# Performance work log

Measured on AMD Instinct MI355X. Metric: run time of the kernel, lower is better.

The kernel has to match this reference:

```python
import jax, jax.numpy as jnp
import numpy as np
import itertools as it
from math import factorial

DIM, N = 3, 30
K = 2 * DIM * N + 1          # 181
P = factorial(N) // factorial(N - DIM)  # 24360
DEMB = DIM * DIM + K         # 190

# permutation index tables (trace-time constants)
_combs = np.array(list(it.permutations(range(N), DIM)), dtype=np.int32)          # (P, DIM)
_rest = np.array([sorted(set(range(N)) - set(map(int, c))) for c in _combs],
                 dtype=np.int32)                                                  # (P, N-DIM)


def setup_inputs() -> dict:
    key = jax.random.key(0)
    k0, k1, k2, k3, k4 = jax.random.split(key, 5)
    return {
        "matrix": jax.random.normal(k0, (DIM, N), dtype=jnp.float32),
        "Ws_in": jax.random.normal(k1, (K, DIM), dtype=jnp.float32),        # inner weights_sort
        "Wd_in": jax.random.normal(k2, (K, N - DIM), dtype=jnp.float32),    # inner weights_dot
        "Ws_out": jax.random.normal(k3, (K, DEMB), dtype=jnp.float32),      # outer weights_sort
        "Wd_out": jax.random.normal(k4, (K, P), dtype=jnp.float32),         # outer weights_dot
    }


def reference(matrix, Ws_in, Wd_in, Ws_out, Wd_out):
    combs = jnp.asarray(_combs)   # (P, DIM)
    rest = jnp.asarray(_rest)     # (P, N-DIM)
    cols = matrix.T               # (N, DIM) -- columns of the cloud as rows

    # UpperGram, batched over all P permutations
    Xd = cols[combs].transpose(0, 2, 1)   # (P, DIM, DIM) selected columns
    Xr = cols[rest].transpose(0, 2, 1)    # (P, DIM, N-DIM) remaining columns (sorted)
    gram = jnp.einsum('pdi,pdj->pij', Xd, Xd)          # Xd^T Xd, (P, DIM, DIM)
    # torch flattens gram.transpose(1,0); gram is exactly symmetric so this equals row-major
    gram_flat = gram.transpose(0, 2, 1).reshape(P, DIM * DIM)
    proj = jnp.einsum('pdi,pdm->pim', Xd, Xr)          # Xd^T Xrest, (P, DIM, N-DIM)

    # inner Embed (non-original branch), batched over P
    sm = jnp.einsum('pim,ki->pmk', proj, Ws_in)        # (P, N-DIM, K)
    sm_sorted = jnp.sort(sm, axis=1)                   # column-wise sort (dim=0 in torch)
    emb = jnp.einsum('km,pmk->pk', Wd_in, sm_sorted)   # diag(Wd @ sorted), (P, K)

    vec = jnp.concatenate([gram_flat, emb], axis=1)    # (P, DEMB); torch's vec before .t()

    # outer Embed (original branch) on mat = vec.T (DEMB, P)
    sm2 = vec @ Ws_out.T                               # mat^T @ Ws^T, (P, K)
    sm2_sorted = jnp.sort(sm2, axis=0)                 # sort over permutation axis
    out = jnp.einsum('kp,pk->k', Wd_out, sm2_sorted)   # diag(Wd @ sorted), (K,)
    return out
```

## Files before the change

kernel.cpp:

```cpp
#include <hip/hip_runtime.h>
#include <hip/hip_bf16.h>

#define DIMK 3
#define NPTS 30
#define KK   181
#define PP   24360
#define DEMB 190
#define VLD  192
#define SNP  24576

typedef __attribute__((ext_vector_type(8))) short bf16x8;
typedef __attribute__((ext_vector_type(4))) float f32x4;
typedef __attribute__((ext_vector_type(2))) __fp16 h2;
typedef __attribute__((ext_vector_type(4))) ushort u16x4;

__device__ __forceinline__ ushort f2bf(float f) {
    unsigned u = __float_as_uint(f);
    u += 0x7FFFu + ((u >> 16) & 1u);
    return (ushort)(u >> 16);
}

__global__ __launch_bounds__(1024, 2) void k_inner(
    const float* __restrict__ M,
    const float* __restrict__ Ws_in,
    const float* __restrict__ Wd_in,
    const float* __restrict__ Wout,
    ushort* __restrict__ Abf,
    ushort* __restrict__ vec)
{
    __shared__ float Gs[NPTS * 32];
    __shared__ float WsS[192 * 3];
    __shared__ float WdS[192 * 28];

    const int tid = threadIdx.x;

    {
        int gid = blockIdx.x * 1024 + tid;
        if (gid < 192 * 192) {
            int k = gid / 192, d = gid - k * 192;
            Abf[gid] = (k < KK && d < DEMB) ? f2bf(Wout[k * DEMB + d]) : (ushort)0;
        }
    }

    for (int i = tid; i < 192 * 3; i += 1024) WsS[i] = (i < KK * 3) ? Ws_in[i] : 0.f;
    for (int i = tid; i < 192 * 28; i += 1024) {
        int k = i / 28, m = i - k * 28;
        WdS[i] = (k < KK && m < 27) ? Wd_in[k * 27 + m] : 0.f;
    }
    for (int e = tid; e < NPTS * 32; e += 1024) {
        int a = e >> 5, b = e & 31;
        Gs[e] = (b < NPTS)
            ? (M[a] * M[b] + M[NPTS + a] * M[NPTS + b] + M[2 * NPTS + a] * M[2 * NPTS + b])
            : 0.f;
    }
    __syncthreads();

    const int wave = __builtin_amdgcn_readfirstlane(tid >> 6);
    const int lane = tid & 63;
    const int wid = blockIdx.x * 16 + wave;
    const int chunk = wid % 3;
    const int pstream = wid / 3;
    const int nstream = (chunk == 2) ? 2730 : 2731;
    const int k = chunk * 64 + lane;

    const float INF = __builtin_inff();
    const bool kvalid = (k < KK);
    const float w0 = WsS[k * 3 + 0];
    const float w1 = WsS[k * 3 + 1];
    const float w2 = WsS[k * 3 + 2];
    const float* wd = WdS + k * 28;

    const int NPAIR = PP / 2;

    for (int t = pstream; t < NPAIR; t += nstream) {
        const int p0 = 2 * t;
        int i0 = p0 / 812;
        int r  = p0 - i0 * 812;
        int i1 = r / 28;
        int i2 = r - i1 * 28;
        int c0 = i0;
        int c1 = i1 + (i1 >= c0 ? 1 : 0);
        int lo = min(c0, c1), hi = max(c0, c1);
        int c2a = i2;
        if (c2a >= lo) c2a++;
        if (c2a >= hi) c2a++;
        int c2b = i2 + 1;
        if (c2b >= lo) c2b++;
        if (c2b >= hi) c2b++;

        ushort* vrow0 = vec + (long)p0 * VLD;
        ushort* vrow1 = vrow0 + VLD;

        if (chunk == 0 && lane < 9) {
            int i = lane / 3, j = lane % 3;
            int cia = (i == 0) ? c0 : ((i == 1) ? c1 : c2a);
            int cja = (j == 0) ? c0 : ((j == 1) ? c1 : c2a);
            vrow0[lane] = f2bf(Gs[(cia << 5) + cja]);
            int cib = (i == 0) ? c0 : ((i == 1) ? c1 : c2b);
            int cjb = (j == 0) ? c0 : ((j == 1) ? c1 : c2b);
            vrow1[lane] = f2bf(Gs[(cib << 5) + cjb]);
        }

        const float* g0 = Gs + (c0 << 5);
        const float* g1 = Gs + (c1 << 5);
        const float* ga = Gs + (c2a << 5);
        const float* gb = Gs + (c2b << 5);
        const unsigned basem = (1u << c0) | (1u << c1);
        const unsigned maska = basem | (1u << c2a);
        const unsigned maskb = basem | (1u << c2b);

        h2 s[30];
#pragma unroll
        for (int q = 0; q < 8; ++q) {
            float4 x0 = *(const float4*)&g0[q * 4];
            float4 x1 = *(const float4*)&g1[q * 4];
            float4 xa = *(const float4*)&ga[q * 4];
            float4 xb = *(const float4*)&gb[q * 4];
            int j0 = q * 4;
            if (j0 + 0 < NPTS) {
                float c = w0 * x0.x + w1 * x1.x;
                float va = w2 * xa.x + c;
                float vb = w2 * xb.x + c;
                va = ((maska >> (j0 + 0)) & 1u) ? INF : va;
                vb = ((maskb >> (j0 + 0)) & 1u) ? INF : vb;
                s[j0 + 0] = __builtin_amdgcn_cvt_pkrtz(va, vb);
            }
            if (j0 + 1 < NPTS) {
                float c = w0 * x0.y + w1 * x1.y;
                float va = w2 * xa.y + c;
                float vb = w2 * xb.y + c;
                va = ((maska >> (j0 + 1)) & 1u) ? INF : va;
                vb = ((maskb >> (j0 + 1)) & 1u) ? INF : vb;
                s[j0 + 1] = __builtin_amdgcn_cvt_pkrtz(va, vb);
            }
            if (j0 + 2 < NPTS) {
                float c = w0 * x0.z + w1 * x1.z;
                float va = w2 * xa.z + c;
                float vb = w2 * xb.z + c;
                va = ((maska >> (j0 + 2)) & 1u) ? INF : va;
                vb = ((maskb >> (j0 + 2)) & 1u) ? INF : vb;
                s[j0 + 2] = __builtin_amdgcn_cvt_pkrtz(va, vb);
            }
            if (j0 + 3 < NPTS) {
                float c = w0 * x0.w + w1 * x1.w;
                float va = w2 * xa.w + c;
                float vb = w2 * xb.w + c;
                va = ((maska >> (j0 + 3)) & 1u) ? INF : va;
                vb = ((maskb >> (j0 + 3)) & 1u) ? INF : vb;
                s[j0 + 3] = __builtin_amdgcn_cvt_pkrtz(va, vb);
            }
        }

#pragma unroll
        for (int pw = 1; pw < 32; pw <<= 1) {
#pragma unroll
            for (int kk = pw; kk >= 1; kk >>= 1) {
#pragma unroll
                for (int j = kk % pw; j + kk < 32; j += 2 * kk) {
#pragma unroll
                    for (int i = 0; i < kk; ++i) {
                        int a = i + j, b = i + j + kk;
                        if (a / (pw * 2) == b / (pw * 2) && b < 30
                            && !(pw == 16 && a == 27)) {
                            h2 x = s[a], y = s[b];
                            s[a] = __builtin_elementwise_min(x, y);
                            s[b] = __builtin_elementwise_max(x, y);
                        }
                    }
                }
            }
        }

        if (kvalid) {
            float emb0 = 0.f, emb1 = 0.f;
#pragma unroll
            for (int j = 0; j < 24; j += 4) {
                float4 w4 = *(const float4*)&wd[j];
                emb0 += w4.x * (float)s[j + 0].x + w4.y * (float)s[j + 1].x
                      + w4.z * (float)s[j + 2].x + w4.w * (float)s[j + 3].x;
                emb1 += w4.x * (float)s[j + 0].y + w4.y * (float)s[j + 1].y
                      + w4.z * (float)s[j + 2].y + w4.w * (float)s[j + 3].y;
            }
            {
                float4 w4 = *(const float4*)&wd[24];
                emb0 += w4.x * (float)s[24].x + w4.y * (float)s[25].x
                      + w4.z * (float)s[26].x;
                emb1 += w4.x * (float)s[24].y + w4.y * (float)s[25].y
                      + w4.z * (float)s[26].y;
            }
            vrow0[9 + k] = f2bf(emb0);
            vrow1[9 + k] = f2bf(emb1);
        } else if (k < 183) {
            vrow0[9 + k] = 0;
            vrow1[9 + k] = 0;
        }
    }
}

__global__ __launch_bounds__(256) void k_gemm(
    const ushort* __restrict__ vecB,
    const ushort* __restrict__ Abf,
    ushort* __restrict__ sm2TP)
{
    const int tid  = threadIdx.x;
    const int bid  = blockIdx.x;
    const int tile = bid >> 2;
    const int qtr  = bid & 3;
    const int wave = tid >> 6;
    const int lane = tid & 63;
    const int n = lane & 15;
    const int quad = lane >> 4;

    const int prow = tile * 64 + wave * 16 + n;
    bf16x8 afrag[6];
    {
        const ushort* row = vecB + (size_t)prow * VLD;
#pragma unroll
        for (int kc = 0; kc < 6; ++kc)
            afrag[kc] = *(const bf16x8*)&row[kc * 32 + quad * 8];
    }

    const int pb = tile * 64 + wave * 16 + quad * 4;

#pragma unroll
    for (int i = 0; i < 3; ++i) {
        const int kt = qtr * 3 + i;
        const int kg = kt * 16 + n;
        f32x4 acc = {0.f, 0.f, 0.f, 0.f};
        const ushort* arow = Abf + kg * 192;
#pragma unroll
        for (int kc = 0; kc < 6; ++kc) {
            bf16x8 bfrag = *(const bf16x8*)&arow[kc * 32 + quad * 8];
            acc = __builtin_amdgcn_mfma_f32_16x16x32_bf16(afrag[kc], bfrag, acc, 0, 0, 0);
        }
        if (kg < KK) {
            u16x4 st;
#pragma unroll
            for (int r = 0; r < 4; ++r) {
                int p = pb + r;
                unsigned e;
                if (p < PP) {
                    unsigned u = __float_as_uint(acc[r]);
                    u = (u & 0x80000000u) ? ~u : (u | 0x80000000u);
                    e = (u + 0x8000u) >> 16;
                } else {
                    e = 0xFFFFu;
                }
                st[r] = (ushort)e;
            }
            *(u16x4*)&sm2TP[(size_t)kg * SNP + pb] = st;
        }
    }
}

__global__ __launch_bounds__(1024, 1) void k_hist(
    const ushort* __restrict__ sm2TP,
    const float* __restrict__ WdOut,
    float* __restrict__ out)
{
    __shared__ float PS[PP + 1];
    __shared__ unsigned hist[16384];
    __shared__ unsigned wred[16];
    __shared__ float fred[16];

    const int tid  = threadIdx.x;
    const int wave = tid >> 6;
    const int lane = tid & 63;
    const int k    = blockIdx.x;

    const ushort* rowU = sm2TP + (size_t)k * SNP;
    const float* wrow  = WdOut + (size_t)k * PP;

#pragma unroll
    for (int j = 0; j < 24; ++j) {
        int i = tid + j * 1024;
        if (i < PP) PS[i] = wrow[i];
    }
    __syncthreads();

    float v[25];
    float csum = 0.f;
    const int cbase = tid * 25;
    if (tid < 975) {
#pragma unroll
        for (int j = 0; j < 25; ++j) {
            int i = cbase + j;
            v[j] = (i < PP) ? PS[i] : 0.f;
            csum += v[j];
        }
    }
    float finc = csum;
#pragma unroll
    for (int off = 1; off < 64; off <<= 1) {
        float o = __shfl_up(finc, off, 64);
        if (lane >= off) finc += o;
    }
    __syncthreads();
    if (lane == 63) fred[wave] = finc;
    __syncthreads();
    float fbase = 0.f;
#pragma unroll
    for (int ww = 0; ww < 16; ++ww) fbase += (ww < wave) ? fred[ww] : 0.f;
    if (tid < 975) {
        float run = fbase + (finc - csum);
#pragma unroll
        for (int j = 0; j < 25; ++j) {
            int i = cbase + j;
            if (i <= PP) PS[i] = run;
            run += v[j];
        }
    }
    __syncthreads();

    float acc = 0.f;
    unsigned below = 0;
    for (int p2 = 0; p2 < 2; ++p2) {
        const unsigned kbase = (unsigned)p2 << 15;

        for (int i = tid; i < 16384; i += 1024) hist[i] = 0u;
        __syncthreads();

        for (int j = 0; j < 24; ++j) {
            unsigned u = rowU[tid + j * 1024];
            unsigned rel = u - kbase;
            if (rel < 32768u) {
                unsigned wd = rel >> 1;
                atomicAdd(&hist[((wd & 15u) << 10) + (wd >> 4)],
                          1u << ((rel & 1u) << 4));
            }
        }
        __syncthreads();

        unsigned w[16];
        unsigned tsum = 0;
#pragma unroll
        for (int i = 0; i < 16; ++i) {
            w[i] = hist[(i << 10) + tid];
            tsum += (w[i] & 0xFFFFu) + (w[i] >> 16);
        }
        unsigned inc = tsum;
#pragma unroll
        for (int off = 1; off < 64; off <<= 1) {
            unsigned o = (unsigned)__shfl_up((int)inc, off, 64);
            if (lane >= off) inc += o;
        }
        if (lane == 63) wred[wave] = inc;
        __syncthreads();
        unsigned wbase = 0, tot = 0;
#pragma unroll
        for (int ww = 0; ww < 16; ++ww) {
            unsigned t = wred[ww];
            tot += t;
            wbase += (ww < wave) ? t : 0u;
        }

        unsigned running = below + wbase + (inc - tsum);
#pragma unroll
        for (int i = 0; i < 16; ++i) {
            unsigned binlo = kbase + (unsigned)tid * 32u + 2u * (unsigned)i;
            unsigned cl = w[i] & 0xFFFFu;
            if (cl) {
                unsigned r1 = min(running, (unsigned)PP);
                unsigned r2 = min(running + cl, (unsigned)PP);
                if (r1 < r2) {
                    unsigned raw16 = (binlo & 0x8000u) ? (binlo & 0x7FFFu)
                                                       : ((~binlo) & 0xFFFFu);
                    acc += __uint_as_float(raw16 << 16) * (PS[r2] - PS[r1]);
                }
            }
            running += cl;
            unsigned ch = w[i] >> 16;
            if (ch) {
                unsigned binhi = binlo + 1u;
                unsigned r1 = min(running, (unsigned)PP);
                unsigned r2 = min(running + ch, (unsigned)PP);
                if (r1 < r2) {
                    unsigned raw16 = (binhi & 0x8000u) ? (binhi & 0x7FFFu)
                                                       : ((~binhi) & 0xFFFFu);
                    acc += __uint_as_float(raw16 << 16) * (PS[r2] - PS[r1]);
                }
            }
            running += ch;
        }
        below += tot;
        __syncthreads();
    }

#pragma unroll
    for (int off = 32; off > 0; off >>= 1)
        acc += __shfl_down(acc, off, 64);
    if (lane == 0) fred[wave] = acc;
    __syncthreads();
    if (tid == 0) {
        float t = 0.f;
#pragma unroll
        for (int ww = 0; ww < 16; ++ww) t += fred[ww];
        out[k] = t;
    }
}

extern "C" void kernel_launch(void* const* d_in, const int* in_sizes, int n_in,
                              void* d_out, int out_size, void* d_ws, size_t ws_size,
                              hipStream_t stream) {
    const float* M      = (const float*)d_in[0];
    const float* Ws_in  = (const float*)d_in[1];
    const float* Wd_in  = (const float*)d_in[2];
    const float* Ws_out = (const float*)d_in[3];
    const float* Wd_out = (const float*)d_in[4];
    float* out = (float*)d_out;

    char* ws = (char*)d_ws;
    ushort* vecB  = (ushort*)ws;
    ushort* sm2TP = (ushort*)(ws + (size_t)PP * VLD * 2);
    ushort* Abf   = (ushort*)(ws + (size_t)PP * VLD * 2 + (size_t)KK * SNP * 2);

    k_inner<<<512, 1024, 0, stream>>>(M, Ws_in, Wd_in, Ws_out, Abf, vecB);

    k_gemm<<<(SNP / 64) * 4, 256, 0, stream>>>(vecB, Abf, sm2TP);

    k_hist<<<KK, 1024, 0, stream>>>(sm2TP, Wd_out, out);
}
```

Before: 165.4 us.

## Replace prefix-sum weighting with counting-sort scatter and direct dot product

The histogram kernel no longer builds a shared-memory prefix sum of the Wd_out row and weights each bin by a difference of prefix values. It turns the histogram into bin start offsets, scatters each bf16 key into its sorted position through a second atomic pass, and then takes a dot product of the sorted values with the weight row, read with vectorized global loads. Keys are loaded once into registers as 4-wide vectors, and the row stride is padded to reduce bank or channel conflicts. The cost is a second round of atomics plus a scattered shared-memory write, in exchange for dropping the serial per-thread scan of the weight row.

```diff
diff --git a/kernel.cpp b/kernel.cpp
--- a/kernel.cpp
+++ b/kernel.cpp
@@ -8,11 +8,13 @@
 #define DEMB 190
 #define VLD  192
 #define SNP  24576
+#define SNPS 24608
 
 typedef __attribute__((ext_vector_type(8))) short bf16x8;
 typedef __attribute__((ext_vector_type(4))) float f32x4;
 typedef __attribute__((ext_vector_type(2))) __fp16 h2;
 typedef __attribute__((ext_vector_type(4))) ushort u16x4;
+typedef __attribute__((ext_vector_type(4))) unsigned u32x4;
 
 __device__ __forceinline__ ushort f2bf(float f) {
     unsigned u = __float_as_uint(f);
@@ -248,7 +250,7 @@
                 }
                 st[r] = (ushort)e;
             }
-            *(u16x4*)&sm2TP[(size_t)kg * SNP + pb] = st;
+            *(u16x4*)&sm2TP[(size_t)kg * SNPS + pb] = st;
         }
     }
 }
@@ -258,8 +260,8 @@
     const float* __restrict__ WdOut,
     float* __restrict__ out)
 {
-    __shared__ float PS[PP + 1];
     __shared__ unsigned hist[16384];
+    __shared__ ushort sv[SNP];
     __shared__ unsigned wred[16];
     __shared__ float fred[16];
 
@@ -268,65 +270,33 @@
     const int lane = tid & 63;
     const int k    = blockIdx.x;
 
-    const ushort* rowU = sm2TP + (size_t)k * SNP;
+    const ushort* rowU = sm2TP + (size_t)k * SNPS;
     const float* wrow  = WdOut + (size_t)k * PP;
 
-#pragma unroll
-    for (int j = 0; j < 24; ++j) {
-        int i = tid + j * 1024;
-        if (i < PP) PS[i] = wrow[i];
-    }
-    __syncthreads();
-
-    float v[25];
-    float csum = 0.f;
-    const int cbase = tid * 25;
-    if (tid < 975) {
-#pragma unroll
-        for (int j = 0; j < 25; ++j) {
-            int i = cbase + j;
-            v[j] = (i < PP) ? PS[i] : 0.f;
-            csum += v[j];
-        }
-    }
-    float finc = csum;
-#pragma unroll
-    for (int off = 1; off < 64; off <<= 1) {
-        float o = __shfl_up(finc, off, 64);
-        if (lane >= off) finc += o;
-    }
-    __syncthreads();
-    if (lane == 63) fred[wave] = finc;
-    __syncthreads();
-    float fbase = 0.f;
-#pragma unroll
-    for (int ww = 0; ww < 16; ++ww) fbase += (ww < wave) ? fred[ww] : 0.f;
-    if (tid < 975) {
-        float run = fbase + (finc - csum);
-#pragma unroll
-        for (int j = 0; j < 25; ++j) {
-            int i = cbase + j;
-            if (i <= PP) PS[i] = run;
-            run += v[j];
-        }
-    }
-    __syncthreads();
-
-    float acc = 0.f;
+    u16x4 kv[6];
+#pragma unroll
+    for (int j = 0; j < 6; ++j)
+        kv[j] = *(const u16x4*)&rowU[tid * 4 + j * 4096];
+
     unsigned below = 0;
     for (int p2 = 0; p2 < 2; ++p2) {
         const unsigned kbase = (unsigned)p2 << 15;
 
-        for (int i = tid; i < 16384; i += 1024) hist[i] = 0u;
+        for (int i = tid; i < 4096; i += 1024)
+            ((u32x4*)hist)[i] = (u32x4){0u, 0u, 0u, 0u};
         __syncthreads();
 
-        for (int j = 0; j < 24; ++j) {
-            unsigned u = rowU[tid + j * 1024];
-            unsigned rel = u - kbase;
-            if (rel < 32768u) {
-                unsigned wd = rel >> 1;
-                atomicAdd(&hist[((wd & 15u) << 10) + (wd >> 4)],
-                          1u << ((rel & 1u) << 4));
+#pragma unroll
+        for (int j = 0; j < 6; ++j) {
+#pragma unroll
+            for (int e = 0; e < 4; ++e) {
+                unsigned u = kv[j][e];
+                unsigned rel = u - kbase;
+                if (rel < 32768u) {
+                    unsigned wd = rel >> 1;
+                    atomicAdd(&hist[((wd & 15u) << 10) + (wd >> 4)],
+                              1u << ((rel & 1u) << 4));
+                }
             }
         }
         __syncthreads();
@@ -357,33 +327,48 @@
         unsigned running = below + wbase + (inc - tsum);
 #pragma unroll
         for (int i = 0; i < 16; ++i) {
-            unsigned binlo = kbase + (unsigned)tid * 32u + 2u * (unsigned)i;
-            unsigned cl = w[i] & 0xFFFFu;
-            if (cl) {
-                unsigned r1 = min(running, (unsigned)PP);
-                unsigned r2 = min(running + cl, (unsigned)PP);
-                if (r1 < r2) {
-                    unsigned raw16 = (binlo & 0x8000u) ? (binlo & 0x7FFFu)
-                                                       : ((~binlo) & 0xFFFFu);
-                    acc += __uint_as_float(raw16 << 16) * (PS[r2] - PS[r1]);
+            unsigned lob = running;
+            running += (w[i] & 0xFFFFu);
+            unsigned hib = running;
+            running += (w[i] >> 16);
+            hist[(i << 10) + tid] = lob | (hib << 16);
+        }
+        __syncthreads();
+
+#pragma unroll
+        for (int j = 0; j < 6; ++j) {
+#pragma unroll
+            for (int e = 0; e < 4; ++e) {
+                unsigned u = kv[j][e];
+                unsigned rel = u - kbase;
+                if (rel < 32768u) {
+                    unsigned wd = rel >> 1;
+                    unsigned sh = (rel & 1u) << 4;
+                    unsigned old = atomicAdd(&hist[((wd & 15u) << 10) + (wd >> 4)],
+                                             1u << sh);
+                    unsigned r = (old >> sh) & 0xFFFFu;
+                    unsigned raw16 = (u & 0x8000u) ? (u & 0x7FFFu)
+                                                   : ((~u) & 0xFFFFu);
+                    sv[r] = (ushort)raw16;
                 }
             }
-            running += cl;
-            unsigned ch = w[i] >> 16;
-            if (ch) {
-                unsigned binhi = binlo + 1u;
-                unsigned r1 = min(running, (unsigned)PP);
-                unsigned r2 = min(running + ch, (unsigned)PP);
-                if (r1 < r2) {
-                    unsigned raw16 = (binhi & 0x8000u) ? (binhi & 0x7FFFu)
-                                                       : ((~binhi) & 0xFFFFu);
-                    acc += __uint_as_float(raw16 << 16) * (PS[r2] - PS[r1]);
-                }
-            }
-            running += ch;
         }
         below += tot;
         __syncthreads();
+    }
+
+    float acc = 0.f;
+#pragma unroll
+    for (int j = 0; j < 6; ++j) {
+        int i4 = tid * 4 + j * 4096;
+        if (i4 < PP) {
+            u16x4 s4 = *(const u16x4*)&sv[i4];
+            float4 w4 = *(const float4*)&wrow[i4];
+            acc += w4.x * __uint_as_float((unsigned)s4[0] << 16)
+                 + w4.y * __uint_as_float((unsigned)s4[1] << 16)
+                 + w4.z * __uint_as_float((unsigned)s4[2] << 16)
+                 + w4.w * __uint_as_float((unsigned)s4[3] << 16);
+        }
     }
 
 #pragma unroll
@@ -411,8 +396,8 @@
 
     char* ws = (char*)d_ws;
     ushort* vecB  = (ushort*)ws;
-    ushort* sm2TP = (ushort*)(ws + (size_t)PP * VLD * 2);
-    ushort* Abf   = (ushort*)(ws + (size_t)PP * VLD * 2 + (size_t)KK * SNP * 2);
+    ushort* Abf   = (ushort*)(ws + (size_t)PP * VLD * 2);
+    ushort* sm2TP = (ushort*)(ws + (size_t)PP * VLD * 2 + (size_t)192 * 192 * 2);
 
     k_inner<<<512, 1024, 0, stream>>>(M, Ws_in, Wd_in, Ws_out, Abf, vecB);
 
```

Measured after the change: 160.4 us (median of 2 runs). 3.1% less time.
